# Kernel optimization log

Measured on AMD Instinct MI355X. Metric: run time of the kernel, lower is better.

## Reference

```python
import jax, jax.numpy as jnp
import numpy as np

N_NODES = 50000
N_EDGES = 800000
NUM_FEATS = 128
HIDDEN = 512
OUT = 2


def setup_inputs() -> dict:
    key = jax.random.key(0)
    k1, k2, k3, k4 = jax.random.split(key, 4)
    X = jax.random.normal(k1, (N_NODES, NUM_FEATS), dtype=jnp.float32)
    edge_index = jax.random.randint(k2, (2, N_EDGES), 0, N_NODES, dtype=jnp.int64)
    W1 = jax.random.normal(k3, (NUM_FEATS, HIDDEN), dtype=jnp.float32) / np.sqrt(NUM_FEATS)
    b1 = jnp.zeros((HIDDEN,), dtype=jnp.float32)
    W2 = jax.random.normal(k4, (HIDDEN, OUT), dtype=jnp.float32) / np.sqrt(HIDDEN)
    b2 = jnp.zeros((OUT,), dtype=jnp.float32)
    return {"X": X, "edge_index": edge_index, "W1": W1, "b1": b1, "W2": W2, "b2": b2}


def _gcn_conv(x, W, b, src, dst, dinv, n):
    # PyG GCNConv: x' = D^{-1/2} (A + I) D^{-1/2} (x W) + b
    xw = x @ W  # [N, C]
    edge_norm = dinv[src] * dinv[dst]  # [E]
    msg = xw[src] * edge_norm[:, None]  # [E, C] gathered messages
    agg = jax.ops.segment_sum(msg, dst, num_segments=n)
    agg = agg + xw * (dinv * dinv)[:, None]  # self-loop contribution
    return agg + b


def reference(X, edge_index, W1, b1, W2, b2):
    n = X.shape[0]
    src, dst = edge_index[0], edge_index[1]
    # degree with self-loops (gcn_norm): deg[i] = in_degree(i) + 1
    deg = jax.ops.segment_sum(jnp.ones_like(dst, dtype=X.dtype), dst, num_segments=n) + 1.0
    dinv = jax.lax.rsqrt(deg)
    h = jax.nn.relu(_gcn_conv(X, W1, b1, src, dst, dinv, n))
    logits = _gcn_conv(h, W2, b2, src, dst, dinv, n)
    # nn.Softmax() on a 2D tensor defaults to dim=1
    return jax.nn.softmax(logits, axis=1)
```

## Files before the change

kernel.cpp:

```cpp
#include <hip/hip_runtime.h>

#define N_FEATS 128
#define HIDDEN 512
#define NPAD 50176
#define ELLW 64
#define NBKT 196
#define SLAB 4608

typedef __attribute__((ext_vector_type(4))) float floatx4;
typedef __attribute__((ext_vector_type(8))) short shortx8;
typedef __attribute__((ext_vector_type(8))) unsigned short ushortx8;

__device__ __forceinline__ unsigned short f2bf(float f) {
    union { float f; unsigned u; } a; a.f = f;
    unsigned r = a.u + 0x7fff + ((a.u >> 16) & 1);
    return (unsigned short)(r >> 16);
}

#define XH_BLOCKS 6250
__global__ __launch_bounds__(256) void k_init(const float* __restrict__ W1,
        unsigned short* __restrict__ w1t, const float* __restrict__ X,
        unsigned short* __restrict__ Xh, int* __restrict__ bcur, int N) {
    int b = blockIdx.x, tid = threadIdx.x;
    if (b < 16) {
        __shared__ unsigned short t[64][65];
        int ki = b >> 3, ni = b & 7;
        #pragma unroll
        for (int i = 0; i < 16; ++i) {
            int idx = tid + i * 256;
            int r = idx >> 6, c = idx & 63;
            t[r][c] = f2bf(W1[(ki * 64 + r) * 512 + ni * 64 + c]);
        }
        __syncthreads();
        #pragma unroll
        for (int i = 0; i < 16; ++i) {
            int idx = tid + i * 256;
            int rn = idx >> 6, ck = idx & 63;
            w1t[(ni * 64 + rn) * 128 + ki * 64 + ck] = t[ck][rn];
        }
    } else if (b == 16) {
        if (tid < 256) bcur[tid] = 0;
    } else {
        int idx = (b - 17) * 256 + tid;
        if (idx < N * 32) {
            float4 v = reinterpret_cast<const float4*>(X)[idx];
            ushort4 o;
            o.x = f2bf(v.x); o.y = f2bf(v.y); o.z = f2bf(v.z); o.w = f2bf(v.w);
            reinterpret_cast<ushort4*>(Xh)[idx] = o;
        }
    }
}

#define PA_EPB 4096
__global__ __launch_bounds__(256) void k_bucketA(const int* __restrict__ src,
        const int* __restrict__ dst, int* __restrict__ bcur,
        unsigned* __restrict__ staging, int E) {
    __shared__ int hist[NBKT];
    __shared__ int base[NBKT];
    int tid = threadIdx.x;
    for (int i = tid; i < NBKT; i += 256) hist[i] = 0;
    __syncthreads();
    #pragma unroll
    for (int i = 0; i < 4; ++i) {
        int e = blockIdx.x * PA_EPB + (i * 256 + tid) * 4;
        if (e + 3 < E) {
            int4 d4 = *reinterpret_cast<const int4*>(dst + e);
            atomicAdd(&hist[d4.x >> 8], 1);
            atomicAdd(&hist[d4.y >> 8], 1);
            atomicAdd(&hist[d4.z >> 8], 1);
            atomicAdd(&hist[d4.w >> 8], 1);
        } else {
            for (int k = 0; k < 4; ++k)
                if (e + k < E) atomicAdd(&hist[dst[e + k] >> 8], 1);
        }
    }
    __syncthreads();
    for (int i = tid; i < NBKT; i += 256) {
        int c = hist[i];
        base[i] = c ? atomicAdd(&bcur[i], c) : 0;
        hist[i] = 0;
    }
    __syncthreads();
    #pragma unroll
    for (int i = 0; i < 4; ++i) {
        int e = blockIdx.x * PA_EPB + (i * 256 + tid) * 4;
        if (e + 3 < E) {
            int4 d4 = *reinterpret_cast<const int4*>(dst + e);
            int4 s4 = *reinterpret_cast<const int4*>(src + e);
            #define PUT(dd, ss) { int bk = (dd) >> 8; int r = atomicAdd(&hist[bk], 1); \
                int pos = base[bk] + r; if (pos < SLAB) \
                staging[(size_t)bk * SLAB + pos] = ((unsigned)(ss) << 8) | (unsigned)((dd) & 255); }
            PUT(d4.x, s4.x) PUT(d4.y, s4.y) PUT(d4.z, s4.z) PUT(d4.w, s4.w)
        } else {
            for (int k = 0; k < 4; ++k)
                if (e + k < E) { int dd = dst[e + k], ss = src[e + k]; PUT(dd, ss) }
            #undef PUT
        }
    }
}

__global__ __launch_bounds__(256) void k_bucketB(const int* __restrict__ bcur,
        const unsigned* __restrict__ staging, int* __restrict__ ell,
        int* __restrict__ cursor, float* __restrict__ dinvs) {
    __shared__ int cur[256];
    int b = blockIdx.x, tid = threadIdx.x;
    cur[tid] = 0;
    __syncthreads();
    int cnt = bcur[b];
    if (cnt > SLAB) cnt = SLAB;
    for (int j = tid; j < cnt; j += 256) {
        unsigned v = staging[(size_t)b * SLAB + j];
        int dl = (int)(v & 255u);
        int s = (int)(v >> 8);
        int pos = atomicAdd(&cur[dl], 1);
        if (pos < ELLW) ell[(size_t)((b << 8) + dl) * ELLW + pos] = s;
    }
    __syncthreads();
    int c = cur[tid];
    cursor[(b << 8) + tid] = c;
    dinvs[(b << 8) + tid] = rsqrtf((float)c + 1.0f);
}

__global__ __launch_bounds__(256) void k_gather(const int* __restrict__ cursor,
        const float* __restrict__ dinvs, const int* __restrict__ ell,
        const unsigned short* __restrict__ Xh, unsigned short* __restrict__ aggAh, int N) {
    int t = blockIdx.x * 256 + threadIdx.x;
    int node = t >> 4;
    int lane = t & 15;
    if (node >= N) return;
    int cnt = cursor[node];
    float dv = dinvs[node];
    int lim = cnt < ELLW ? cnt : ELLW;
    const ushortx8* Xv = reinterpret_cast<const ushortx8*>(Xh);
    #define BF(x) ({ union { unsigned u; float f; } _c; _c.u = (unsigned)(x) << 16; _c.f; })
    union U8 { ushortx8 v; unsigned short s[8]; };
    U8 sv; sv.v = Xv[(size_t)node * 16 + lane];
    float a[8];
    #pragma unroll
    for (int k = 0; k < 8; ++k) a[k] = dv * BF(sv.s[k]);
    const int* row = ell + (size_t)node * ELLW;
    int j = 0;
    int4 nxt;
    if (lim >= 4) nxt = *reinterpret_cast<const int4*>(row);
    for (; j + 4 <= lim; j += 4) {
        int4 s4 = nxt;
        if (j + 8 <= lim) nxt = *reinterpret_cast<const int4*>(row + j + 4);
        float w0 = dinvs[s4.x], w1 = dinvs[s4.y], w2 = dinvs[s4.z], w3 = dinvs[s4.w];
        U8 u0, u1, u2, u3;
        u0.v = Xv[(size_t)s4.x * 16 + lane];
        u1.v = Xv[(size_t)s4.y * 16 + lane];
        u2.v = Xv[(size_t)s4.z * 16 + lane];
        u3.v = Xv[(size_t)s4.w * 16 + lane];
        #pragma unroll
        for (int k = 0; k < 8; ++k)
            a[k] += w0 * BF(u0.s[k]) + w1 * BF(u1.s[k]) + w2 * BF(u2.s[k]) + w3 * BF(u3.s[k]);
    }
    for (; j < lim; ++j) {
        int s = row[j];
        float w = dinvs[s];
        U8 u; u.v = Xv[(size_t)s * 16 + lane];
        #pragma unroll
        for (int k = 0; k < 8; ++k) a[k] += w * BF(u.s[k]);
    }
    #undef BF
    union { ushortx8 v; unsigned short s[8]; } o;
    #pragma unroll
    for (int k = 0; k < 8; ++k) o.s[k] = f2bf(a[k] * dv);
    reinterpret_cast<ushortx8*>(aggAh)[(size_t)node * 16 + lane] = o.v;
}

__global__ __launch_bounds__(256) void k_fused_mfma(
        const unsigned short* __restrict__ aggAh, const unsigned short* __restrict__ w1t,
        const float* __restrict__ b1, const float* __restrict__ W2,
        const float* __restrict__ dinvs, float2* __restrict__ lps, int N) {
    __shared__ unsigned short As[128][136];
    __shared__ unsigned short Bs[128][136];
    __shared__ float b1s[HIDDEN];
    __shared__ float W2s[HIDDEN * 2];

    const int tid = threadIdx.x;
    const int wave = tid >> 6;
    const int lane = tid & 63;
    const int quad = lane >> 4;
    const int l16 = lane & 15;
    const int m0 = blockIdx.x * 128;

    for (int i = tid; i < HIDDEN; i += 256) b1s[i] = b1[i];
    for (int i = tid; i < HIDDEN * 2; i += 256) W2s[i] = W2[i];

    #pragma unroll
    for (int it = 0; it < 8; ++it) {
        int flat = (tid + it * 256) * 8;
        int r = flat >> 7, c = flat & 127;
        int gm = m0 + r;
        shortx8 v = {0, 0, 0, 0, 0, 0, 0, 0};
        if (gm < N) v = *reinterpret_cast<const shortx8*>(aggAh + (size_t)gm * 128 + c);
        *reinterpret_cast<shortx8*>(&As[r][c]) = v;
    }

    float accL0[2][4], accL1[2][4];
    #pragma unroll
    for (int s = 0; s < 2; ++s)
        #pragma unroll
        for (int r = 0; r < 4; ++r) { accL0[s][r] = 0.f; accL1[s][r] = 0.f; }

    for (int n0 = 0; n0 < HIDDEN; n0 += 128) {
        #pragma unroll
        for (int it = 0; it < 8; ++it) {
            int flat = (tid + it * 256) * 8;
            int r = flat >> 7, c = flat & 127;
            *reinterpret_cast<shortx8*>(&Bs[r][c]) =
                *reinterpret_cast<const shortx8*>(w1t + (size_t)(n0 + r) * 128 + c);
        }
        __syncthreads();

        floatx4 acc[2][8];
        #pragma unroll
        for (int s = 0; s < 2; ++s)
            #pragma unroll
            for (int nt = 0; nt < 8; ++nt) acc[s][nt] = (floatx4){0.f, 0.f, 0.f, 0.f};

        #pragma unroll
        for (int ks = 0; ks < 4; ++ks) {
            shortx8 af0 = *reinterpret_cast<const shortx8*>(&As[wave * 32 + l16][ks * 32 + quad * 8]);
            shortx8 af1 = *reinterpret_cast<const shortx8*>(&As[wave * 32 + 16 + l16][ks * 32 + quad * 8]);
            #pragma unroll
            for (int nt = 0; nt < 8; ++nt) {
                shortx8 bf = *reinterpret_cast<const shortx8*>(&Bs[nt * 16 + l16][ks * 32 + quad * 8]);
                acc[0][nt] = __builtin_amdgcn_mfma_f32_16x16x32_bf16(af0, bf, acc[0][nt], 0, 0, 0);
                acc[1][nt] = __builtin_amdgcn_mfma_f32_16x16x32_bf16(af1, bf, acc[1][nt], 0, 0, 0);
            }
        }

        #pragma unroll
        for (int nt = 0; nt < 8; ++nt) {
            int col = n0 + nt * 16 + l16;
            float bb = b1s[col];
            float w20 = W2s[col * 2 + 0];
            float w21 = W2s[col * 2 + 1];
            #pragma unroll
            for (int s = 0; s < 2; ++s) {
                #pragma unroll
                for (int r = 0; r < 4; ++r) {
                    float h = acc[s][nt][r] + bb;
                    h = h > 0.f ? h : 0.f;
                    accL0[s][r] += h * w20;
                    accL1[s][r] += h * w21;
                }
            }
        }
        __syncthreads();
    }

    #pragma unroll
    for (int off = 1; off < 16; off <<= 1) {
        #pragma unroll
        for (int s = 0; s < 2; ++s)
            #pragma unroll
            for (int r = 0; r < 4; ++r) {
                accL0[s][r] += __shfl_xor(accL0[s][r], off);
                accL1[s][r] += __shfl_xor(accL1[s][r], off);
            }
    }
    if (l16 == 0) {
        #pragma unroll
        for (int s = 0; s < 2; ++s)
            #pragma unroll
            for (int r = 0; r < 4; ++r) {
                int gm = m0 + wave * 32 + s * 16 + quad * 4 + r;
                if (gm < N) {
                    float dv = dinvs[gm];
                    lps[gm] = make_float2(dv * accL0[s][r], dv * accL1[s][r]);
                }
            }
    }
}

__global__ __launch_bounds__(256) void k_final(const int* __restrict__ cursor,
        const float* __restrict__ dinvs, const int* __restrict__ ell,
        const float2* __restrict__ lps, const float* __restrict__ b2,
        float* __restrict__ out, int N) {
    int t = blockIdx.x * 256 + threadIdx.x;
    int node = t >> 3;
    int lane = t & 7;
    if (node >= N) return;
    int cnt = cursor[node];
    int lim = cnt < ELLW ? cnt : ELLW;
    const int* row = ell + (size_t)node * ELLW;
    float a0 = 0.f, a1 = 0.f;
    for (int j = lane; j < lim; j += 8) {
        float2 v = lps[row[j]];
        a0 += v.x;
        a1 += v.y;
    }
    #pragma unroll
    for (int off = 1; off < 8; off <<= 1) {
        a0 += __shfl_xor(a0, off);
        a1 += __shfl_xor(a1, off);
    }
    if (lane == 0) {
        float dv = dinvs[node];
        float2 self = lps[node];
        float l0 = dv * (a0 + self.x) + b2[0];
        float l1 = dv * (a1 + self.y) + b2[1];
        float m = fmaxf(l0, l1);
        float e0 = __expf(l0 - m), e1 = __expf(l1 - m);
        float inv = 1.0f / (e0 + e1);
        out[(size_t)node * 2 + 0] = e0 * inv;
        out[(size_t)node * 2 + 1] = e1 * inv;
    }
}

extern "C" void kernel_launch(void* const* d_in, const int* in_sizes, int n_in,
                              void* d_out, int out_size, void* d_ws, size_t ws_size,
                              hipStream_t stream) {
    const float* X  = (const float*)d_in[0];
    const int* ei   = (const int*)d_in[1];
    const float* W1 = (const float*)d_in[2];
    const float* b1 = (const float*)d_in[3];
    const float* W2 = (const float*)d_in[4];
    const float* b2 = (const float*)d_in[5];
    float* out = (float*)d_out;

    const int N = in_sizes[0] / N_FEATS;
    const int E = in_sizes[1] / 2;
    const int* src = ei;
    const int* dst = ei + E;

    int* cursor = (int*)d_ws;
    int* bcur   = cursor + NPAD;
    int* ell    = bcur + 256;
    float2* lps = (float2*)(ell + (size_t)NPAD * ELLW);
    float* dinvs = (float*)(lps + NPAD);
    unsigned short* w1t = (unsigned short*)(dinvs + NPAD);
    unsigned short* Xh  = w1t + 512 * 128;
    unsigned* staging = (unsigned*)(Xh + (size_t)NPAD * 128);
    unsigned short* aggAh = (unsigned short*)staging;

    k_init    <<<17 + XH_BLOCKS, 256, 0, stream>>>(W1, w1t, X, Xh, bcur, N);
    k_bucketA <<<(E + PA_EPB - 1) / PA_EPB, 256, 0, stream>>>(src, dst, bcur, staging, E);
    k_bucketB <<<NBKT, 256, 0, stream>>>(bcur, staging, ell, cursor, dinvs);
    k_gather  <<<((size_t)N * 16 + 255) / 256, 256, 0, stream>>>(cursor, dinvs, ell, Xh, aggAh, N);
    k_fused_mfma<<<(N + 127) / 128, 256, 0, stream>>>(aggAh, w1t, b1, W2, dinvs, lps, N);
    k_final   <<<((size_t)N * 8 + 255) / 256, 256, 0, stream>>>(cursor, dinvs, ell, lps, b2, out, N);
}
```

Before: 166.7 us.

## Fuse edge bucketing into init kernel and split gather into column halves

The bucketA edge-partitioning pass is merged into the init kernel as extra blocks, so conversion of X and W1 runs alongside the bucketing. The bcur reset becomes a hipMemsetAsync, which saves one dependent kernel launch. The gather kernel now uses 8 lanes per node and two grid halves that each cover 64 feature columns, so each neighbor's row is read in two separate passes. This is meant to improve cache locality per half, at the cost of reading the index and weight data twice.

```diff
diff --git a/kernel.cpp b/kernel.cpp
--- a/kernel.cpp
+++ b/kernel.cpp
@@ -6,6 +6,10 @@
 #define ELLW 64
 #define NBKT 196
 #define SLAB 4608
+#define PA_EPB 4096
+#define PA_BLOCKS 196
+#define XH_BLOCKS 6250
+#define GB_HALF 1563
 
 typedef __attribute__((ext_vector_type(4))) float floatx4;
 typedef __attribute__((ext_vector_type(8))) short shortx8;
@@ -17,14 +21,58 @@
     return (unsigned short)(r >> 16);
 }
 
-#define XH_BLOCKS 6250
-__global__ __launch_bounds__(256) void k_init(const float* __restrict__ W1,
+__global__ __launch_bounds__(256) void k_initA(const float* __restrict__ W1,
         unsigned short* __restrict__ w1t, const float* __restrict__ X,
-        unsigned short* __restrict__ Xh, int* __restrict__ bcur, int N) {
+        unsigned short* __restrict__ Xh, const int* __restrict__ src,
+        const int* __restrict__ dst, int* __restrict__ bcur,
+        unsigned* __restrict__ staging, int E, int N) {
     int b = blockIdx.x, tid = threadIdx.x;
-    if (b < 16) {
+    if (b < PA_BLOCKS) {
+        __shared__ int hist[NBKT];
+        __shared__ int base[NBKT];
+        for (int i = tid; i < NBKT; i += 256) hist[i] = 0;
+        __syncthreads();
+        #pragma unroll
+        for (int i = 0; i < 4; ++i) {
+            int e = b * PA_EPB + (i * 256 + tid) * 4;
+            if (e + 3 < E) {
+                int4 d4 = *reinterpret_cast<const int4*>(dst + e);
+                atomicAdd(&hist[d4.x >> 8], 1);
+                atomicAdd(&hist[d4.y >> 8], 1);
+                atomicAdd(&hist[d4.z >> 8], 1);
+                atomicAdd(&hist[d4.w >> 8], 1);
+            } else {
+                for (int k = 0; k < 4; ++k)
+                    if (e + k < E) atomicAdd(&hist[dst[e + k] >> 8], 1);
+            }
+        }
+        __syncthreads();
+        for (int i = tid; i < NBKT; i += 256) {
+            int c = hist[i];
+            base[i] = c ? atomicAdd(&bcur[i], c) : 0;
+            hist[i] = 0;
+        }
+        __syncthreads();
+        #pragma unroll
+        for (int i = 0; i < 4; ++i) {
+            int e = b * PA_EPB + (i * 256 + tid) * 4;
+            if (e + 3 < E) {
+                int4 d4 = *reinterpret_cast<const int4*>(dst + e);
+                int4 s4 = *reinterpret_cast<const int4*>(src + e);
+                #define PUT(dd, ss) { int bk = (dd) >> 8; int r = atomicAdd(&hist[bk], 1); \
+                    int pos = base[bk] + r; if (pos < SLAB) \
+                    staging[(size_t)bk * SLAB + pos] = ((unsigned)(ss) << 8) | (unsigned)((dd) & 255); }
+                PUT(d4.x, s4.x) PUT(d4.y, s4.y) PUT(d4.z, s4.z) PUT(d4.w, s4.w)
+            } else {
+                for (int k = 0; k < 4; ++k)
+                    if (e + k < E) { int dd = dst[e + k], ss = src[e + k]; PUT(dd, ss) }
+                #undef PUT
+            }
+        }
+    } else if (b < PA_BLOCKS + 16) {
         __shared__ unsigned short t[64][65];
-        int ki = b >> 3, ni = b & 7;
+        int bb = b - PA_BLOCKS;
+        int ki = bb >> 3, ni = bb & 7;
         #pragma unroll
         for (int i = 0; i < 16; ++i) {
             int idx = tid + i * 256;
@@ -38,63 +86,13 @@
             int rn = idx >> 6, ck = idx & 63;
             w1t[(ni * 64 + rn) * 128 + ki * 64 + ck] = t[ck][rn];
         }
-    } else if (b == 16) {
-        if (tid < 256) bcur[tid] = 0;
     } else {
-        int idx = (b - 17) * 256 + tid;
+        int idx = (b - PA_BLOCKS - 16) * 256 + tid;
         if (idx < N * 32) {
             float4 v = reinterpret_cast<const float4*>(X)[idx];
             ushort4 o;
             o.x = f2bf(v.x); o.y = f2bf(v.y); o.z = f2bf(v.z); o.w = f2bf(v.w);
             reinterpret_cast<ushort4*>(Xh)[idx] = o;
-        }
-    }
-}
-
-#define PA_EPB 4096
-__global__ __launch_bounds__(256) void k_bucketA(const int* __restrict__ src,
-        const int* __restrict__ dst, int* __restrict__ bcur,
-        unsigned* __restrict__ staging, int E) {
-    __shared__ int hist[NBKT];
-    __shared__ int base[NBKT];
-    int tid = threadIdx.x;
-    for (int i = tid; i < NBKT; i += 256) hist[i] = 0;
-    __syncthreads();
-    #pragma unroll
-    for (int i = 0; i < 4; ++i) {
-        int e = blockIdx.x * PA_EPB + (i * 256 + tid) * 4;
-        if (e + 3 < E) {
-            int4 d4 = *reinterpret_cast<const int4*>(dst + e);
-            atomicAdd(&hist[d4.x >> 8], 1);
-            atomicAdd(&hist[d4.y >> 8], 1);
-            atomicAdd(&hist[d4.z >> 8], 1);
-            atomicAdd(&hist[d4.w >> 8], 1);
-        } else {
-            for (int k = 0; k < 4; ++k)
-                if (e + k < E) atomicAdd(&hist[dst[e + k] >> 8], 1);
-        }
-    }
-    __syncthreads();
-    for (int i = tid; i < NBKT; i += 256) {
-        int c = hist[i];
-        base[i] = c ? atomicAdd(&bcur[i], c) : 0;
-        hist[i] = 0;
-    }
-    __syncthreads();
-    #pragma unroll
-    for (int i = 0; i < 4; ++i) {
-        int e = blockIdx.x * PA_EPB + (i * 256 + tid) * 4;
-        if (e + 3 < E) {
-            int4 d4 = *reinterpret_cast<const int4*>(dst + e);
-            int4 s4 = *reinterpret_cast<const int4*>(src + e);
-            #define PUT(dd, ss) { int bk = (dd) >> 8; int r = atomicAdd(&hist[bk], 1); \
-                int pos = base[bk] + r; if (pos < SLAB) \
-                staging[(size_t)bk * SLAB + pos] = ((unsigned)(ss) << 8) | (unsigned)((dd) & 255); }
-            PUT(d4.x, s4.x) PUT(d4.y, s4.y) PUT(d4.z, s4.z) PUT(d4.w, s4.w)
-        } else {
-            for (int k = 0; k < 4; ++k)
-                if (e + k < E) { int dd = dst[e + k], ss = src[e + k]; PUT(dd, ss) }
-            #undef PUT
         }
     }
 }
@@ -124,17 +122,20 @@
 __global__ __launch_bounds__(256) void k_gather(const int* __restrict__ cursor,
         const float* __restrict__ dinvs, const int* __restrict__ ell,
         const unsigned short* __restrict__ Xh, unsigned short* __restrict__ aggAh, int N) {
-    int t = blockIdx.x * 256 + threadIdx.x;
-    int node = t >> 4;
-    int lane = t & 15;
+    int b = blockIdx.x;
+    int half = (b >= GB_HALF) ? 1 : 0;
+    int t = (b - half * GB_HALF) * 256 + threadIdx.x;
+    int node = t >> 3;
+    int lane = t & 7;
     if (node >= N) return;
     int cnt = cursor[node];
     float dv = dinvs[node];
     int lim = cnt < ELLW ? cnt : ELLW;
+    int coff = half * 8 + lane;
     const ushortx8* Xv = reinterpret_cast<const ushortx8*>(Xh);
     #define BF(x) ({ union { unsigned u; float f; } _c; _c.u = (unsigned)(x) << 16; _c.f; })
     union U8 { ushortx8 v; unsigned short s[8]; };
-    U8 sv; sv.v = Xv[(size_t)node * 16 + lane];
+    U8 sv; sv.v = Xv[(size_t)node * 16 + coff];
     float a[8];
     #pragma unroll
     for (int k = 0; k < 8; ++k) a[k] = dv * BF(sv.s[k]);
@@ -147,10 +148,10 @@
         if (j + 8 <= lim) nxt = *reinterpret_cast<const int4*>(row + j + 4);
         float w0 = dinvs[s4.x], w1 = dinvs[s4.y], w2 = dinvs[s4.z], w3 = dinvs[s4.w];
         U8 u0, u1, u2, u3;
-        u0.v = Xv[(size_t)s4.x * 16 + lane];
-        u1.v = Xv[(size_t)s4.y * 16 + lane];
-        u2.v = Xv[(size_t)s4.z * 16 + lane];
-        u3.v = Xv[(size_t)s4.w * 16 + lane];
+        u0.v = Xv[(size_t)s4.x * 16 + coff];
+        u1.v = Xv[(size_t)s4.y * 16 + coff];
+        u2.v = Xv[(size_t)s4.z * 16 + coff];
+        u3.v = Xv[(size_t)s4.w * 16 + coff];
         #pragma unroll
         for (int k = 0; k < 8; ++k)
             a[k] += w0 * BF(u0.s[k]) + w1 * BF(u1.s[k]) + w2 * BF(u2.s[k]) + w3 * BF(u3.s[k]);
@@ -158,7 +159,7 @@
     for (; j < lim; ++j) {
         int s = row[j];
         float w = dinvs[s];
-        U8 u; u.v = Xv[(size_t)s * 16 + lane];
+        U8 u; u.v = Xv[(size_t)s * 16 + coff];
         #pragma unroll
         for (int k = 0; k < 8; ++k) a[k] += w * BF(u.s[k]);
     }
@@ -166,7 +167,7 @@
     union { ushortx8 v; unsigned short s[8]; } o;
     #pragma unroll
     for (int k = 0; k < 8; ++k) o.s[k] = f2bf(a[k] * dv);
-    reinterpret_cast<ushortx8*>(aggAh)[(size_t)node * 16 + lane] = o.v;
+    reinterpret_cast<ushortx8*>(aggAh)[(size_t)node * 16 + coff] = o.v;
 }
 
 __global__ __launch_bounds__(256) void k_fused_mfma(
@@ -337,10 +338,11 @@
     unsigned* staging = (unsigned*)(Xh + (size_t)NPAD * 128);
     unsigned short* aggAh = (unsigned short*)staging;
 
-    k_init    <<<17 + XH_BLOCKS, 256, 0, stream>>>(W1, w1t, X, Xh, bcur, N);
-    k_bucketA <<<(E + PA_EPB - 1) / PA_EPB, 256, 0, stream>>>(src, dst, bcur, staging, E);
+    hipMemsetAsync(bcur, 0, 256 * sizeof(int), stream);
+    k_initA   <<<PA_BLOCKS + 16 + XH_BLOCKS, 256, 0, stream>>>(
+                  W1, w1t, X, Xh, src, dst, bcur, staging, E, N);
     k_bucketB <<<NBKT, 256, 0, stream>>>(bcur, staging, ell, cursor, dinvs);
-    k_gather  <<<((size_t)N * 16 + 255) / 256, 256, 0, stream>>>(cursor, dinvs, ell, Xh, aggAh, N);
+    k_gather  <<<2 * GB_HALF, 256, 0, stream>>>(cursor, dinvs, ell, Xh, aggAh, N);
     k_fused_mfma<<<(N + 127) / 128, 256, 0, stream>>>(aggAh, w1t, b1, W2, dinvs, lps, N);
     k_final   <<<((size_t)N * 8 + 255) / 256, 256, 0, stream>>>(cursor, dinvs, ell, lps, b2, out, N);
 }
```

Measured after the change: 165.7 us. Within noise of the previous version (-0.6%).
